# Kernel tuning notes

Measured on AMD Instinct MI355X. Metric: run time of the kernel, lower is better.

The kernel has to match this reference:

```python
import jax, jax.numpy as jnp
import numpy as np

P_NULL = 1e-4


def _neg_mean_sqdist(x, c):
    # x: [B, D], c: [D, K] -> [B, K] = -mean_D (x - c)^2, computed via expansion
    # (same math as torch's (x[:,None]-c.T[None]).square().neg().mean(-1),
    #  avoids materializing a [B,K,D] tensor)
    D = x.shape[-1]
    x2 = jnp.sum(x * x, axis=-1, keepdims=True)          # [B,1]
    c2 = jnp.sum(c * c, axis=0)[None, :]                 # [1,K]
    xc = x @ c                                           # [B,K]
    return -(x2 - 2.0 * xc + c2) / D


def setup_inputs() -> dict:
    key = jax.random.key(0)
    k1, k2, k3 = jax.random.split(key, 3)
    B, G, E, K = 4096, 64, 32, 8192
    images = jax.random.normal(k1, (B, G), dtype=jnp.float32)
    # params mimic nn.Linear weight init scale (kaiming-uniform-ish); exact init irrelevant for math
    xa = jax.random.normal(k2, (G, K), dtype=jnp.float32) * (1.0 / np.sqrt(G))
    xb = jax.random.normal(k3, (E, K), dtype=jnp.float32) * (1.0 / np.sqrt(E))
    return {"images": images, "xa": xa, "xb": xb, "n_step": 4}


def reference(images, xa, xb, n_step):
    B = images.shape[0]
    log_pnull = jnp.log(jnp.float32(P_NULL))

    # ---- encode ----
    lpik = _neg_mean_sqdist(images, xa)                   # [B,K]
    z = jax.nn.softmax(lpik, axis=-1) @ xb.T              # [B,E]
    for _ in range(n_step):
        lxqik = _neg_mean_sqdist(z, xb)                   # [B,K]
        lxq = jnp.concatenate(
            [lxqik, jnp.full((B, 1), log_pnull, dtype=lxqik.dtype)], axis=1)
        lxq = jax.nn.log_softmax(lxq, axis=-1)            # [B,K+1]
        ljp = lpik + lxq[:, :-1]                          # [B,K]
        xp = jax.nn.softmax(ljp, axis=-1)                 # [B,K]
        z = z + 0.1 * (xp @ xb.T - z)                     # [B,E]

    # ---- decode (ret='rec') ----
    xqik = jnp.exp(_neg_mean_sqdist(z, xb))               # [B,K]
    xqik = xqik / (P_NULL + jnp.sum(xqik, axis=-1, keepdims=True))
    y = xqik @ xa.T                                       # [B,G]
    return y
```

## Files before the change

kernel.cpp:

```cpp
#include <hip/hip_runtime.h>
#include <hip/hip_fp16.h>
#include <math.h>

static constexpr int Gd = 64;
static constexpr int Ed = 32;
static constexpr int Kd = 8192;
static constexpr int R  = 4;
static constexpr int T  = 1024;
static constexpr int NW = 16;
static constexpr int NP = 4;
static constexpr int CS = 2 * T;
static constexpr int EQ = 2;
static constexpr int NEQ = Ed / EQ;
static constexpr float PNULLF = 1e-4f;

template<int CTRL, int RMASK>
__device__ __forceinline__ float dpp_add(float v) {
  int t = __builtin_amdgcn_update_dpp(0, __builtin_bit_cast(int, v), CTRL, RMASK, 0xf, true);
  return v + __builtin_bit_cast(float, t);
}
template<int CTRL, int RMASK>
__device__ __forceinline__ float dpp_fmax(float v) {
  int t = __builtin_amdgcn_update_dpp(__builtin_bit_cast(int, -__builtin_inff()),
                                      __builtin_bit_cast(int, v), CTRL, RMASK, 0xf, false);
  return fmaxf(v, __builtin_bit_cast(float, t));
}
__device__ __forceinline__ float wave_sum(float v) {
  v = dpp_add<0x111, 0xf>(v);
  v = dpp_add<0x112, 0xf>(v);
  v = dpp_add<0x114, 0xf>(v);
  v = dpp_add<0x118, 0xf>(v);
  v = dpp_add<0x142, 0xa>(v);
  v = dpp_add<0x143, 0xc>(v);
  return v;
}
__device__ __forceinline__ float half_sum(float v) {
  v = dpp_add<0x111, 0xf>(v);
  v = dpp_add<0x112, 0xf>(v);
  v = dpp_add<0x114, 0xf>(v);
  v = dpp_add<0x118, 0xf>(v);
  v = dpp_add<0x142, 0xa>(v);
  return v;
}
__device__ __forceinline__ float wave_max(float v) {
  v = dpp_fmax<0x111, 0xf>(v);
  v = dpp_fmax<0x112, 0xf>(v);
  v = dpp_fmax<0x114, 0xf>(v);
  v = dpp_fmax<0x118, 0xf>(v);
  v = dpp_fmax<0x142, 0xa>(v);
  v = dpp_fmax<0x143, 0xc>(v);
  return v;
}

template<bool HW>
__device__ __forceinline__ float2 ldw(const void* p, size_t idx) {
  if constexpr (HW) {
    __half2 h = *reinterpret_cast<const __half2*>(reinterpret_cast<const __half*>(p) + idx);
    return __half22float2(h);
  } else {
    return *reinterpret_cast<const float2*>(reinterpret_cast<const float*>(p) + idx);
  }
}
template<bool HW>
__device__ __forceinline__ float4 ld4w(const void* p, size_t idx) {
  if constexpr (HW) {
    const __half2* ph = reinterpret_cast<const __half2*>(reinterpret_cast<const __half*>(p) + idx);
    float2 a = __half22float2(ph[0]);
    float2 b = __half22float2(ph[1]);
    return make_float4(a.x, a.y, b.x, b.y);
  } else {
    return *reinterpret_cast<const float4*>(reinterpret_cast<const float*>(p) + idx);
  }
}

static constexpr int OFF_LP   = 0;
static constexpr int OFF_IMG  = 32768;
static constexpr int OFF_ZT   = 33024;
static constexpr int OFF_WRD  = 33152;
static constexpr int OFF_MLD  = 35264;
static constexpr int OFF_SLD  = 35268;
static constexpr int OFF_Z2   = 35272;
static constexpr int OFF_X2   = 35276;
static constexpr int SMEM_FLOATS = 35280;

template<bool HW>
__global__ __attribute__((amdgpu_flat_work_group_size(T, T), amdgpu_waves_per_eu(4, 4)))
void glgae_fused(
    const float* __restrict__ images,
    const void*  __restrict__ xaP,
    const void*  __restrict__ xbP,
    const float* __restrict__ c2aP,
    const float* __restrict__ cb2P,
    const int*   __restrict__ nstep_p,
    float* __restrict__ out)
{
  extern __shared__ float sm[];
  float* LP  = sm + OFF_LP;
  float* IMG = sm + OFF_IMG;
  float* ZT  = sm + OFF_ZT;
  float* WRD = sm + OFF_WRD;
  float* MLD = sm + OFF_MLD;
  float* SLD = sm + OFF_SLD;
  float* Z2L = sm + OFF_Z2;
  float* X2L = sm + OFF_X2;

  const int tid  = (int)threadIdx.x;
  const int lane = tid & 63;
  const int wv   = tid >> 6;
  const int rowbase = (int)blockIdx.x * R;
  const int nstep = nstep_p[0];
  const int kb0 = tid * 2;

  if (tid < Gd * R) {
    int g = tid >> 2, r = tid & 3;
    IMG[g * R + r] = images[(size_t)(rowbase + r) * Gd + g];
  }
  __syncthreads();
  if (tid < R) {
    float s = 0.f;
    #pragma unroll
    for (int g = 0; g < Gd; ++g) { float v = IMG[g * R + tid]; s = fmaf(v, v, s); }
    X2L[tid] = s;
  }

  {
    float xk[R][NP][2];
    float c2l[NP][2];
    #pragma unroll
    for (int r = 0; r < R; ++r)
      #pragma unroll
      for (int i = 0; i < NP; ++i) { xk[r][i][0] = 0.f; xk[r][i][1] = 0.f; }
    #pragma unroll
    for (int i = 0; i < NP; ++i) { c2l[i][0] = 0.f; c2l[i][1] = 0.f; }

    #pragma unroll 2
    for (int g = 0; g < Gd; ++g) {
      float4 imv4 = *reinterpret_cast<const float4*>(&IMG[g * R]);
      float im[4] = {imv4.x, imv4.y, imv4.z, imv4.w};
      #pragma unroll
      for (int i = 0; i < NP; ++i) {
        float2 w = ldw<HW>(xaP, (size_t)g * Kd + i * CS + kb0);
        if constexpr (!HW) {
          c2l[i][0] = fmaf(w.x, w.x, c2l[i][0]);
          c2l[i][1] = fmaf(w.y, w.y, c2l[i][1]);
        }
        #pragma unroll
        for (int r = 0; r < R; ++r) {
          xk[r][i][0] = fmaf(im[r], w.x, xk[r][i][0]);
          xk[r][i][1] = fmaf(im[r], w.y, xk[r][i][1]);
        }
      }
    }
    __syncthreads();

    float mx[R] = {-__builtin_inff(), -__builtin_inff(), -__builtin_inff(), -__builtin_inff()};
    float x2r[R];
    #pragma unroll
    for (int r = 0; r < R; ++r) x2r[r] = X2L[r];
    #pragma unroll
    for (int i = 0; i < NP; ++i) {
      float cx, cy;
      if constexpr (HW) {
        float2 c = *reinterpret_cast<const float2*>(&c2aP[i * CS + kb0]);
        cx = c.x; cy = c.y;
      } else { cx = c2l[i][0]; cy = c2l[i][1]; }
      #pragma unroll
      for (int r = 0; r < R; ++r) {
        float v0 = (2.f * xk[r][i][0] - x2r[r] - cx) * (1.f / 64.f);
        float v1 = (2.f * xk[r][i][1] - x2r[r] - cy) * (1.f / 64.f);
        mx[r] = fmaxf(mx[r], fmaxf(v0, v1));
        *reinterpret_cast<float2*>(&LP[r * Kd + i * CS + kb0]) = make_float2(v0, v1);
      }
    }
    #pragma unroll
    for (int r = 0; r < R; ++r) mx[r] = wave_max(mx[r]);
    if (lane == 63) {
      #pragma unroll
      for (int r = 0; r < R; ++r) WRD[wv * 132 + 128 + r] = mx[r];
    }
    __syncthreads();
    if (tid < R) {
      float m = -__builtin_inff();
      #pragma unroll
      for (int w = 0; w < NW; ++w) m = fmaxf(m, WRD[w * 132 + 128 + tid]);
      MLD[tid] = m;
    }
    __syncthreads();
  }

  {
    float p[R][NP][2];
    float s1[R] = {0.f, 0.f, 0.f, 0.f};
    #pragma unroll
    for (int i = 0; i < NP; ++i) {
      #pragma unroll
      for (int r = 0; r < R; ++r) {
        float2 l = *reinterpret_cast<const float2*>(&LP[r * Kd + i * CS + kb0]);
        float m = MLD[r];
        float p0 = __expf(l.x - m);
        float p1 = __expf(l.y - m);
        p[r][i][0] = p0; p[r][i][1] = p1;
        s1[r] += p0 + p1;
      }
    }

    float c2v[NP][2];
    #pragma unroll
    for (int i = 0; i < NP; ++i) { c2v[i][0] = 0.f; c2v[i][1] = 0.f; }

    #pragma unroll 1
    for (int eq = 0; eq < NEQ; ++eq) {
      float zacc[R][EQ];
      #pragma unroll
      for (int r = 0; r < R; ++r)
        #pragma unroll
        for (int e2 = 0; e2 < EQ; ++e2) zacc[r][e2] = 0.f;

      #pragma unroll
      for (int i = 0; i < NP; ++i) {
        #pragma unroll
        for (int e2 = 0; e2 < EQ; ++e2) {
          int e = eq * EQ + e2;
          float2 w = ldw<HW>(xbP, (size_t)e * Kd + i * CS + kb0);
          if constexpr (!HW) {
            c2v[i][0] = fmaf(w.x, w.x, c2v[i][0]);
            c2v[i][1] = fmaf(w.y, w.y, c2v[i][1]);
          }
          #pragma unroll
          for (int r = 0; r < R; ++r) {
            zacc[r][e2] = fmaf(p[r][i][0], w.x, zacc[r][e2]);
            zacc[r][e2] = fmaf(p[r][i][1], w.y, zacc[r][e2]);
          }
        }
      }
      #pragma unroll
      for (int r = 0; r < R; ++r)
        #pragma unroll
        for (int e2 = 0; e2 < EQ; ++e2) zacc[r][e2] = wave_sum(zacc[r][e2]);
      if (lane == 63) {
        #pragma unroll
        for (int r = 0; r < R; ++r)
          #pragma unroll
          for (int e2 = 0; e2 < EQ; ++e2)
            WRD[wv * 132 + r * 32 + eq * EQ + e2] = zacc[r][e2];
      }
    }

    #pragma unroll
    for (int r = 0; r < R; ++r) s1[r] = wave_sum(s1[r]);
    if (lane == 63) {
      #pragma unroll
      for (int r = 0; r < R; ++r) WRD[wv * 132 + 128 + r] = s1[r];
    }

    #pragma unroll
    for (int i = 0; i < NP; ++i) {
      float cx, cy;
      if constexpr (HW) {
        float2 c = *reinterpret_cast<const float2*>(&cb2P[i * CS + kb0]);
        cx = c.x; cy = c.y;
      } else { cx = c2v[i][0]; cy = c2v[i][1]; }
      #pragma unroll
      for (int r = 0; r < R; ++r) {
        float2 l = *reinterpret_cast<const float2*>(&LP[r * Kd + i * CS + kb0]);
        l.x -= cx * (1.f / 32.f);
        l.y -= cy * (1.f / 32.f);
        *reinterpret_cast<float2*>(&LP[r * Kd + i * CS + kb0]) = l;
      }
    }

    __syncthreads();
    if (tid < 128) {
      int r = tid >> 5, e = tid & 31;
      float zs = 0.f, ss = 0.f;
      #pragma unroll
      for (int w = 0; w < NW; ++w) { zs += WRD[w * 132 + r * 32 + e]; ss += WRD[w * 132 + 128 + r]; }
      float zn = zs / ss;
      ZT[e * R + r] = zn;
      float q = half_sum(zn * zn);
      if ((lane & 31) == 31) Z2L[r] = q;
    }
    __syncthreads();
  }

  for (int st = 0; st < nstep; ++st) {
    float al[R];
    #pragma unroll
    for (int r = 0; r < R; ++r) al[r] = fmaf(Z2L[r], -(1.f / 32.f), -MLD[r]);

    float up[R][NP][2];
    #pragma unroll
    for (int r = 0; r < R; ++r)
      #pragma unroll
      for (int i = 0; i < NP; ++i) { up[r][i][0] = 0.f; up[r][i][1] = 0.f; }
    #pragma unroll 2
    for (int e = 0; e < Ed; ++e) {
      float4 zv = *reinterpret_cast<const float4*>(&ZT[e * R]);
      float z4[4] = {zv.x, zv.y, zv.z, zv.w};
      #pragma unroll
      for (int i = 0; i < NP; ++i) {
        float2 w = ldw<HW>(xbP, (size_t)e * Kd + i * CS + kb0);
        #pragma unroll
        for (int r = 0; r < R; ++r) {
          up[r][i][0] = fmaf(z4[r], w.x, up[r][i][0]);
          up[r][i][1] = fmaf(z4[r], w.y, up[r][i][1]);
        }
      }
    }

    float s2[R] = {0.f, 0.f, 0.f, 0.f};
    #pragma unroll
    for (int i = 0; i < NP; ++i) {
      #pragma unroll
      for (int r = 0; r < R; ++r) {
        float2 l = *reinterpret_cast<const float2*>(&LP[r * Kd + i * CS + kb0]);
        float p0 = __expf(l.x + al[r] + up[r][i][0] * (1.f / 16.f));
        float p1 = __expf(l.y + al[r] + up[r][i][1] * (1.f / 16.f));
        up[r][i][0] = p0; up[r][i][1] = p1;
        s2[r] += p0 + p1;
      }
    }

    #pragma unroll 1
    for (int eq = 0; eq < NEQ; ++eq) {
      float zacc[R][EQ];
      #pragma unroll
      for (int r = 0; r < R; ++r)
        #pragma unroll
        for (int e2 = 0; e2 < EQ; ++e2) zacc[r][e2] = 0.f;

      #pragma unroll
      for (int i = 0; i < NP; ++i) {
        #pragma unroll
        for (int e2 = 0; e2 < EQ; ++e2) {
          int e = eq * EQ + e2;
          float2 w = ldw<HW>(xbP, (size_t)e * Kd + i * CS + kb0);
          #pragma unroll
          for (int r = 0; r < R; ++r) {
            zacc[r][e2] = fmaf(up[r][i][0], w.x, zacc[r][e2]);
            zacc[r][e2] = fmaf(up[r][i][1], w.y, zacc[r][e2]);
          }
        }
      }
      #pragma unroll
      for (int r = 0; r < R; ++r)
        #pragma unroll
        for (int e2 = 0; e2 < EQ; ++e2) zacc[r][e2] = wave_sum(zacc[r][e2]);
      if (lane == 63) {
        #pragma unroll
        for (int r = 0; r < R; ++r)
          #pragma unroll
          for (int e2 = 0; e2 < EQ; ++e2)
            WRD[wv * 132 + r * 32 + eq * EQ + e2] = zacc[r][e2];
      }
    }

    #pragma unroll
    for (int r = 0; r < R; ++r) s2[r] = wave_sum(s2[r]);
    if (lane == 63) {
      #pragma unroll
      for (int r = 0; r < R; ++r) WRD[wv * 132 + 128 + r] = s2[r];
    }
    __syncthreads();
    if (tid < 128) {
      int r = tid >> 5, e = tid & 31;
      float zs = 0.f, ss = 0.f;
      #pragma unroll
      for (int w = 0; w < NW; ++w) { zs += WRD[w * 132 + r * 32 + e]; ss += WRD[w * 132 + 128 + r]; }
      float zn = fmaf(0.1f, zs / ss, 0.9f * ZT[e * R + r]);
      ZT[e * R + r] = zn;
      float q = half_sum(zn * zn);
      if ((lane & 31) == 31) Z2L[r] = q;
    }
    __syncthreads();
  }

  {
    float u[R][NP][2];
    float cw2[NP][2];
    #pragma unroll
    for (int r = 0; r < R; ++r)
      #pragma unroll
      for (int i = 0; i < NP; ++i) { u[r][i][0] = 0.f; u[r][i][1] = 0.f; }
    #pragma unroll
    for (int i = 0; i < NP; ++i) { cw2[i][0] = 0.f; cw2[i][1] = 0.f; }

    #pragma unroll 2
    for (int e = 0; e < Ed; ++e) {
      float4 zv = *reinterpret_cast<const float4*>(&ZT[e * R]);
      float z4[4] = {zv.x, zv.y, zv.z, zv.w};
      #pragma unroll
      for (int i = 0; i < NP; ++i) {
        float2 w = ldw<HW>(xbP, (size_t)e * Kd + i * CS + kb0);
        if constexpr (!HW) {
          cw2[i][0] = fmaf(w.x, w.x, cw2[i][0]);
          cw2[i][1] = fmaf(w.y, w.y, cw2[i][1]);
        }
        #pragma unroll
        for (int r = 0; r < R; ++r) {
          u[r][i][0] = fmaf(z4[r], w.x, u[r][i][0]);
          u[r][i][1] = fmaf(z4[r], w.y, u[r][i][1]);
        }
      }
    }

    float s3[R] = {0.f, 0.f, 0.f, 0.f};
    float nz2[R];
    #pragma unroll
    for (int r = 0; r < R; ++r) nz2[r] = Z2L[r] * -(1.f / 32.f);
    #pragma unroll
    for (int i = 0; i < NP; ++i) {
      float cx, cy;
      if constexpr (HW) {
        float2 c = *reinterpret_cast<const float2*>(&cb2P[i * CS + kb0]);
        cx = c.x; cy = c.y;
      } else { cx = cw2[i][0]; cy = cw2[i][1]; }
      #pragma unroll
      for (int r = 0; r < R; ++r) {
        float e0 = __expf(nz2[r] + u[r][i][0] * (1.f / 16.f) - cx * (1.f / 32.f));
        float e1 = __expf(nz2[r] + u[r][i][1] * (1.f / 16.f) - cy * (1.f / 32.f));
        *reinterpret_cast<float2*>(&LP[r * Kd + i * CS + kb0]) = make_float2(e0, e1);
        s3[r] += e0 + e1;
      }
    }
    #pragma unroll
    for (int r = 0; r < R; ++r) s3[r] = wave_sum(s3[r]);
    if (lane == 63) {
      #pragma unroll
      for (int r = 0; r < R; ++r) WRD[wv * 132 + 128 + r] = s3[r];
    }
    __syncthreads();
    if (tid < R) {
      float s = 0.f;
      #pragma unroll
      for (int w = 0; w < NW; ++w) s += WRD[w * 132 + 128 + tid];
      SLD[tid] = 1.f / (PNULLF + s);
    }
    __syncthreads();
  }

  {
    float inv[R];
    #pragma unroll
    for (int r = 0; r < R; ++r) inv[r] = SLD[r];
    float acc[R][4];
    #pragma unroll
    for (int r = 0; r < R; ++r)
      #pragma unroll
      for (int gi = 0; gi < 4; ++gi) acc[r][gi] = 0.f;

    #pragma unroll 2
    for (int c = 0; c < 32; ++c) {
      float xq[R][4];
      #pragma unroll
      for (int r = 0; r < R; ++r) {
        float4 q = *reinterpret_cast<const float4*>(&LP[r * Kd + c * 256 + lane * 4]);
        xq[r][0] = q.x; xq[r][1] = q.y; xq[r][2] = q.z; xq[r][3] = q.w;
      }
      #pragma unroll
      for (int gi = 0; gi < 4; ++gi) {
        int g = gi * NW + wv;
        float4 wa = ld4w<HW>(xaP, (size_t)g * Kd + c * 256 + lane * 4);
        #pragma unroll
        for (int r = 0; r < R; ++r) {
          acc[r][gi] = fmaf(xq[r][0], wa.x, acc[r][gi]);
          acc[r][gi] = fmaf(xq[r][1], wa.y, acc[r][gi]);
          acc[r][gi] = fmaf(xq[r][2], wa.z, acc[r][gi]);
          acc[r][gi] = fmaf(xq[r][3], wa.w, acc[r][gi]);
        }
      }
    }
    #pragma unroll
    for (int r = 0; r < R; ++r)
      #pragma unroll
      for (int gi = 0; gi < 4; ++gi) acc[r][gi] = wave_sum(acc[r][gi]);
    if (lane == 63) {
      #pragma unroll
      for (int r = 0; r < R; ++r)
        #pragma unroll
        for (int gi = 0; gi < 4; ++gi)
          out[(size_t)(rowbase + r) * Gd + gi * NW + wv] = acc[r][gi] * inv[r];
    }
  }
}

__global__ __launch_bounds__(256) void convert_w(
    const float* __restrict__ xa, const float* __restrict__ xb,
    __half* __restrict__ xah, __half* __restrict__ xbh,
    float* __restrict__ c2a, float* __restrict__ cb2)
{
  int k = (int)(blockIdx.x * blockDim.x + threadIdx.x);
  if (k >= Kd) return;
  float s = 0.f;
  #pragma unroll 4
  for (int g = 0; g < Gd; ++g) {
    float v = xa[(size_t)g * Kd + k];
    xah[(size_t)g * Kd + k] = __float2half(v);
    s = fmaf(v, v, s);
  }
  c2a[k] = s;
  s = 0.f;
  #pragma unroll 4
  for (int e = 0; e < Ed; ++e) {
    float v = xb[(size_t)e * Kd + k];
    xbh[(size_t)e * Kd + k] = __float2half(v);
    s = fmaf(v, v, s);
  }
  cb2[k] = s;
}

extern "C" void kernel_launch(void* const* d_in, const int* in_sizes, int n_in,
                              void* d_out, int out_size, void* d_ws, size_t ws_size,
                              hipStream_t stream) {
  const float* images = (const float*)d_in[0];
  const float* xa     = (const float*)d_in[1];
  const float* xb     = (const float*)d_in[2];
  const int*   nstep  = (const int*)d_in[3];
  float* out = (float*)d_out;

  const size_t smem = (size_t)SMEM_FLOATS * sizeof(float);
  const size_t need = (size_t)(Gd + Ed) * Kd * sizeof(__half) + (size_t)2 * Kd * sizeof(float);

  if (ws_size >= need) {
    __half* xah = (__half*)d_ws;
    __half* xbh = xah + (size_t)Gd * Kd;
    float*  c2a = (float*)(xbh + (size_t)Ed * Kd);
    float*  cb2 = c2a + Kd;
    hipLaunchKernelGGL(convert_w, dim3(Kd / 256), dim3(256), 0, stream,
                       xa, xb, xah, xbh, c2a, cb2);
    (void)hipFuncSetAttribute((const void*)glgae_fused<true>,
                              hipFuncAttributeMaxDynamicSharedMemorySize, (int)smem);
    hipLaunchKernelGGL(glgae_fused<true>, dim3(4096 / R), dim3(T), smem, stream,
                       images, (const void*)xah, (const void*)xbh, c2a, cb2, nstep, out);
  } else {
    (void)hipFuncSetAttribute((const void*)glgae_fused<false>,
                              hipFuncAttributeMaxDynamicSharedMemorySize, (int)smem);
    hipLaunchKernelGGL(glgae_fused<false>, dim3(4096 / R), dim3(T), smem, stream,
                       images, (const void*)xa, (const void*)xb,
                       (const float*)nullptr, (const float*)nullptr, nstep, out);
  }
}
```

Measured before the change: 838.1 us.

## Use packed fp16 dot2 instructions and pair-interleaved weights in fused kernel

Adds a new half-precision path that packs activations (image, z, probabilities) into fp16 pairs and accumulates with v_dot2 fp16->fp32 instructions against weights pre-interleaved in pairs along the reduction dimension. The fused iterative z update is restructured to work directly on packed probabilities, and the decode stores exp values as fp16 in shared memory. This halves the FMA instruction count and shared/global bytes per product, at the cost of rounding activations and probabilities to fp16 and extra workspace for the interleaved weight copies.

```diff
diff --git a/kernel.cpp b/kernel.cpp
--- a/kernel.cpp
+++ b/kernel.cpp
@@ -10,9 +10,9 @@
 static constexpr int NW = 16;
 static constexpr int NP = 4;
 static constexpr int CS = 2 * T;
-static constexpr int EQ = 2;
-static constexpr int NEQ = Ed / EQ;
 static constexpr float PNULLF = 1e-4f;
+
+typedef _Float16 h2v __attribute__((ext_vector_type(2)));
 
 template<int CTRL, int RMASK>
 __device__ __forceinline__ float dpp_add(float v) {
@@ -52,26 +52,30 @@
   return v;
 }
 
-template<bool HW>
-__device__ __forceinline__ float2 ldw(const void* p, size_t idx) {
-  if constexpr (HW) {
-    __half2 h = *reinterpret_cast<const __half2*>(reinterpret_cast<const __half*>(p) + idx);
-    return __half22float2(h);
-  } else {
-    return *reinterpret_cast<const float2*>(reinterpret_cast<const float*>(p) + idx);
-  }
-}
-template<bool HW>
-__device__ __forceinline__ float4 ld4w(const void* p, size_t idx) {
-  if constexpr (HW) {
-    const __half2* ph = reinterpret_cast<const __half2*>(reinterpret_cast<const __half*>(p) + idx);
-    float2 a = __half22float2(ph[0]);
-    float2 b = __half22float2(ph[1]);
-    return make_float4(a.x, a.y, b.x, b.y);
-  } else {
-    return *reinterpret_cast<const float4*>(reinterpret_cast<const float*>(p) + idx);
-  }
-}
+__device__ __forceinline__ float fdot2(h2v a, h2v b, float c) {
+#if defined(__has_builtin)
+#if __has_builtin(__builtin_amdgcn_fdot2)
+  return __builtin_amdgcn_fdot2(a, b, c, false);
+#else
+  return fmaf((float)a.x, (float)b.x, fmaf((float)a.y, (float)b.y, c));
+#endif
+#else
+  return fmaf((float)a.x, (float)b.x, fmaf((float)a.y, (float)b.y, c));
+#endif
+}
+__device__ __forceinline__ h2v pkh(float x, float y) {
+#if defined(__has_builtin)
+#if __has_builtin(__builtin_amdgcn_cvt_pkrtz)
+  return __builtin_bit_cast(h2v, __builtin_amdgcn_cvt_pkrtz(x, y));
+#else
+  h2v h; h.x = (_Float16)x; h.y = (_Float16)y; return h;
+#endif
+#else
+  h2v h; h.x = (_Float16)x; h.y = (_Float16)y; return h;
+#endif
+}
+__device__ __forceinline__ h2v bch(unsigned int u) { return __builtin_bit_cast(h2v, u); }
+__device__ __forceinline__ unsigned int hbits(h2v h) { return __builtin_bit_cast(unsigned int, h); }
 
 static constexpr int OFF_LP   = 0;
 static constexpr int OFF_IMG  = 32768;
@@ -83,12 +87,13 @@
 static constexpr int OFF_X2   = 35276;
 static constexpr int SMEM_FLOATS = 35280;
 
-template<bool HW>
 __global__ __attribute__((amdgpu_flat_work_group_size(T, T), amdgpu_waves_per_eu(4, 4)))
-void glgae_fused(
+void glgae_h2(
     const float* __restrict__ images,
-    const void*  __restrict__ xaP,
-    const void*  __restrict__ xbP,
+    const __half* __restrict__ xah,
+    const __half* __restrict__ xbh,
+    const unsigned int* __restrict__ xai,
+    const unsigned int* __restrict__ xbi,
     const float* __restrict__ c2aP,
     const float* __restrict__ cb2P,
     const int*   __restrict__ nstep_p,
@@ -103,6 +108,7 @@
   float* SLD = sm + OFF_SLD;
   float* Z2L = sm + OFF_Z2;
   float* X2L = sm + OFF_X2;
+  unsigned int* LPH = reinterpret_cast<unsigned int*>(LP);
 
   const int tid  = (int)threadIdx.x;
   const int lane = tid & 63;
@@ -110,6 +116,369 @@
   const int rowbase = (int)blockIdx.x * R;
   const int nstep = nstep_p[0];
   const int kb0 = tid * 2;
+  const int kp0 = tid;
+
+  if (tid < Gd * R) {
+    int g = tid >> 2, r = tid & 3;
+    IMG[g * R + r] = images[(size_t)(rowbase + r) * Gd + g];
+  }
+  __syncthreads();
+  if (tid < R) {
+    float s = 0.f;
+    #pragma unroll
+    for (int g = 0; g < Gd; ++g) { float v = IMG[g * R + tid]; s = fmaf(v, v, s); }
+    X2L[tid] = s;
+  }
+  __syncthreads();
+
+  {
+    float xk[R][NP][2];
+    #pragma unroll
+    for (int r = 0; r < R; ++r)
+      #pragma unroll
+      for (int i = 0; i < NP; ++i) { xk[r][i][0] = 0.f; xk[r][i][1] = 0.f; }
+
+    #pragma unroll 1
+    for (int gp = 0; gp < Gd / 2; ++gp) {
+      float4 ia = *reinterpret_cast<const float4*>(&IMG[(2 * gp) * R]);
+      float4 ib = *reinterpret_cast<const float4*>(&IMG[(2 * gp + 1) * R]);
+      h2v imh[4] = {pkh(ia.x, ib.x), pkh(ia.y, ib.y), pkh(ia.z, ib.z), pkh(ia.w, ib.w)};
+      #pragma unroll
+      for (int i = 0; i < NP; ++i) {
+        uint2 w = *reinterpret_cast<const uint2*>(xai + (size_t)gp * Kd + i * CS + kb0);
+        h2v w0 = bch(w.x), w1 = bch(w.y);
+        #pragma unroll
+        for (int r = 0; r < R; ++r) {
+          xk[r][i][0] = fdot2(imh[r], w0, xk[r][i][0]);
+          xk[r][i][1] = fdot2(imh[r], w1, xk[r][i][1]);
+        }
+      }
+    }
+
+    float mx[R] = {-__builtin_inff(), -__builtin_inff(), -__builtin_inff(), -__builtin_inff()};
+    float x2r[R];
+    #pragma unroll
+    for (int r = 0; r < R; ++r) x2r[r] = X2L[r];
+    #pragma unroll
+    for (int i = 0; i < NP; ++i) {
+      float2 c = *reinterpret_cast<const float2*>(&c2aP[i * CS + kb0]);
+      #pragma unroll
+      for (int r = 0; r < R; ++r) {
+        float v0 = (2.f * xk[r][i][0] - x2r[r] - c.x) * (1.f / 64.f);
+        float v1 = (2.f * xk[r][i][1] - x2r[r] - c.y) * (1.f / 64.f);
+        mx[r] = fmaxf(mx[r], fmaxf(v0, v1));
+        *reinterpret_cast<float2*>(&LP[r * Kd + i * CS + kb0]) = make_float2(v0, v1);
+      }
+    }
+    #pragma unroll
+    for (int r = 0; r < R; ++r) mx[r] = wave_max(mx[r]);
+    if (lane == 63) {
+      #pragma unroll
+      for (int r = 0; r < R; ++r) WRD[wv * 132 + 128 + r] = mx[r];
+    }
+    __syncthreads();
+    if (tid < R) {
+      float m = -__builtin_inff();
+      #pragma unroll
+      for (int w = 0; w < NW; ++w) m = fmaxf(m, WRD[w * 132 + 128 + tid]);
+      MLD[tid] = m;
+    }
+    __syncthreads();
+  }
+
+  const unsigned int* xbhU = reinterpret_cast<const unsigned int*>(xbh);
+  h2v ph[R][NP];
+
+  {
+    float s1[R] = {0.f, 0.f, 0.f, 0.f};
+    #pragma unroll
+    for (int i = 0; i < NP; ++i) {
+      #pragma unroll
+      for (int r = 0; r < R; ++r) {
+        float2 l = *reinterpret_cast<const float2*>(&LP[r * Kd + i * CS + kb0]);
+        float m = MLD[r];
+        float p0 = __expf(l.x - m);
+        float p1 = __expf(l.y - m);
+        s1[r] += p0 + p1;
+        ph[r][i] = pkh(p0, p1);
+      }
+    }
+
+    #pragma unroll 1
+    for (int eq = 0; eq < 8; ++eq) {
+      float acc[R][4];
+      #pragma unroll
+      for (int r = 0; r < R; ++r)
+        #pragma unroll
+        for (int e2 = 0; e2 < 4; ++e2) acc[r][e2] = 0.f;
+      #pragma unroll
+      for (int i = 0; i < NP; ++i) {
+        #pragma unroll
+        for (int e2 = 0; e2 < 4; ++e2) {
+          int e = eq * 4 + e2;
+          h2v w = bch(xbhU[(size_t)e * (Kd / 2) + i * (CS / 2) + kp0]);
+          #pragma unroll
+          for (int r = 0; r < R; ++r) acc[r][e2] = fdot2(ph[r][i], w, acc[r][e2]);
+        }
+      }
+      #pragma unroll
+      for (int r = 0; r < R; ++r)
+        #pragma unroll
+        for (int e2 = 0; e2 < 4; ++e2) acc[r][e2] = wave_sum(acc[r][e2]);
+      if (lane == 63) {
+        #pragma unroll
+        for (int r = 0; r < R; ++r)
+          #pragma unroll
+          for (int e2 = 0; e2 < 4; ++e2)
+            WRD[wv * 132 + r * 32 + eq * 4 + e2] = acc[r][e2];
+      }
+    }
+
+    #pragma unroll
+    for (int r = 0; r < R; ++r) s1[r] = wave_sum(s1[r]);
+    if (lane == 63) {
+      #pragma unroll
+      for (int r = 0; r < R; ++r) WRD[wv * 132 + 128 + r] = s1[r];
+    }
+
+    #pragma unroll
+    for (int i = 0; i < NP; ++i) {
+      float2 c = *reinterpret_cast<const float2*>(&cb2P[i * CS + kb0]);
+      #pragma unroll
+      for (int r = 0; r < R; ++r) {
+        float2 l = *reinterpret_cast<const float2*>(&LP[r * Kd + i * CS + kb0]);
+        l.x -= c.x * (1.f / 32.f);
+        l.y -= c.y * (1.f / 32.f);
+        *reinterpret_cast<float2*>(&LP[r * Kd + i * CS + kb0]) = l;
+      }
+    }
+
+    __syncthreads();
+    if (tid < 128) {
+      int r = tid >> 5, e = tid & 31;
+      float zs = 0.f, ss = 0.f;
+      #pragma unroll
+      for (int w = 0; w < NW; ++w) { zs += WRD[w * 132 + r * 32 + e]; ss += WRD[w * 132 + 128 + r]; }
+      float zn = zs / ss;
+      ZT[e * R + r] = zn;
+      float q = half_sum(zn * zn);
+      if ((lane & 31) == 31) Z2L[r] = q;
+    }
+    __syncthreads();
+  }
+
+  for (int st = 0; st < nstep; ++st) {
+    float al[R];
+    #pragma unroll
+    for (int r = 0; r < R; ++r) al[r] = fmaf(Z2L[r], -(1.f / 32.f), -MLD[r]);
+
+    float u[R][NP][2];
+    #pragma unroll
+    for (int r = 0; r < R; ++r)
+      #pragma unroll
+      for (int i = 0; i < NP; ++i) { u[r][i][0] = 0.f; u[r][i][1] = 0.f; }
+    #pragma unroll 1
+    for (int ep = 0; ep < Ed / 2; ++ep) {
+      float4 za = *reinterpret_cast<const float4*>(&ZT[(2 * ep) * R]);
+      float4 zb = *reinterpret_cast<const float4*>(&ZT[(2 * ep + 1) * R]);
+      h2v zh[4] = {pkh(za.x, zb.x), pkh(za.y, zb.y), pkh(za.z, zb.z), pkh(za.w, zb.w)};
+      #pragma unroll
+      for (int i = 0; i < NP; ++i) {
+        uint2 w = *reinterpret_cast<const uint2*>(xbi + (size_t)ep * Kd + i * CS + kb0);
+        h2v w0 = bch(w.x), w1 = bch(w.y);
+        #pragma unroll
+        for (int r = 0; r < R; ++r) {
+          u[r][i][0] = fdot2(zh[r], w0, u[r][i][0]);
+          u[r][i][1] = fdot2(zh[r], w1, u[r][i][1]);
+        }
+      }
+    }
+
+    float s2[R] = {0.f, 0.f, 0.f, 0.f};
+    #pragma unroll
+    for (int i = 0; i < NP; ++i) {
+      #pragma unroll
+      for (int r = 0; r < R; ++r) {
+        float2 l = *reinterpret_cast<const float2*>(&LP[r * Kd + i * CS + kb0]);
+        float p0 = __expf(l.x + al[r] + u[r][i][0] * (1.f / 16.f));
+        float p1 = __expf(l.y + al[r] + u[r][i][1] * (1.f / 16.f));
+        s2[r] += p0 + p1;
+        ph[r][i] = pkh(p0, p1);
+      }
+    }
+
+    #pragma unroll 1
+    for (int eq = 0; eq < 8; ++eq) {
+      float acc[R][4];
+      #pragma unroll
+      for (int r = 0; r < R; ++r)
+        #pragma unroll
+        for (int e2 = 0; e2 < 4; ++e2) acc[r][e2] = 0.f;
+      #pragma unroll
+      for (int i = 0; i < NP; ++i) {
+        #pragma unroll
+        for (int e2 = 0; e2 < 4; ++e2) {
+          int e = eq * 4 + e2;
+          h2v w = bch(xbhU[(size_t)e * (Kd / 2) + i * (CS / 2) + kp0]);
+          #pragma unroll
+          for (int r = 0; r < R; ++r) acc[r][e2] = fdot2(ph[r][i], w, acc[r][e2]);
+        }
+      }
+      #pragma unroll
+      for (int r = 0; r < R; ++r)
+        #pragma unroll
+        for (int e2 = 0; e2 < 4; ++e2) acc[r][e2] = wave_sum(acc[r][e2]);
+      if (lane == 63) {
+        #pragma unroll
+        for (int r = 0; r < R; ++r)
+          #pragma unroll
+          for (int e2 = 0; e2 < 4; ++e2)
+            WRD[wv * 132 + r * 32 + eq * 4 + e2] = acc[r][e2];
+      }
+    }
+
+    #pragma unroll
+    for (int r = 0; r < R; ++r) s2[r] = wave_sum(s2[r]);
+    if (lane == 63) {
+      #pragma unroll
+      for (int r = 0; r < R; ++r) WRD[wv * 132 + 128 + r] = s2[r];
+    }
+    __syncthreads();
+    if (tid < 128) {
+      int r = tid >> 5, e = tid & 31;
+      float zs = 0.f, ss = 0.f;
+      #pragma unroll
+      for (int w = 0; w < NW; ++w) { zs += WRD[w * 132 + r * 32 + e]; ss += WRD[w * 132 + 128 + r]; }
+      float zn = fmaf(0.1f, zs / ss, 0.9f * ZT[e * R + r]);
+      ZT[e * R + r] = zn;
+      float q = half_sum(zn * zn);
+      if ((lane & 31) == 31) Z2L[r] = q;
+    }
+    __syncthreads();
+  }
+
+  {
+    float u[R][NP][2];
+    #pragma unroll
+    for (int r = 0; r < R; ++r)
+      #pragma unroll
+      for (int i = 0; i < NP; ++i) { u[r][i][0] = 0.f; u[r][i][1] = 0.f; }
+    #pragma unroll 1
+    for (int ep = 0; ep < Ed / 2; ++ep) {
+      float4 za = *reinterpret_cast<const float4*>(&ZT[(2 * ep) * R]);
+      float4 zb = *reinterpret_cast<const float4*>(&ZT[(2 * ep + 1) * R]);
+      h2v zh[4] = {pkh(za.x, zb.x), pkh(za.y, zb.y), pkh(za.z, zb.z), pkh(za.w, zb.w)};
+      #pragma unroll
+      for (int i = 0; i < NP; ++i) {
+        uint2 w = *reinterpret_cast<const uint2*>(xbi + (size_t)ep * Kd + i * CS + kb0);
+        h2v w0 = bch(w.x), w1 = bch(w.y);
+        #pragma unroll
+        for (int r = 0; r < R; ++r) {
+          u[r][i][0] = fdot2(zh[r], w0, u[r][i][0]);
+          u[r][i][1] = fdot2(zh[r], w1, u[r][i][1]);
+        }
+      }
+    }
+
+    float s3[R] = {0.f, 0.f, 0.f, 0.f};
+    float nz2[R];
+    #pragma unroll
+    for (int r = 0; r < R; ++r) nz2[r] = Z2L[r] * -(1.f / 32.f);
+    __syncthreads();
+    #pragma unroll
+    for (int i = 0; i < NP; ++i) {
+      float2 c = *reinterpret_cast<const float2*>(&cb2P[i * CS + kb0]);
+      #pragma unroll
+      for (int r = 0; r < R; ++r) {
+        float e0 = __expf(nz2[r] + u[r][i][0] * (1.f / 16.f) - c.x * (1.f / 32.f));
+        float e1 = __expf(nz2[r] + u[r][i][1] * (1.f / 16.f) - c.y * (1.f / 32.f));
+        LPH[r * (Kd / 2) + i * (CS / 2) + kp0] = hbits(pkh(e0, e1));
+        s3[r] += e0 + e1;
+      }
+    }
+    #pragma unroll
+    for (int r = 0; r < R; ++r) s3[r] = wave_sum(s3[r]);
+    if (lane == 63) {
+      #pragma unroll
+      for (int r = 0; r < R; ++r) WRD[wv * 132 + 128 + r] = s3[r];
+    }
+    __syncthreads();
+    if (tid < R) {
+      float s = 0.f;
+      #pragma unroll
+      for (int w = 0; w < NW; ++w) s += WRD[w * 132 + 128 + tid];
+      SLD[tid] = 1.f / (PNULLF + s);
+    }
+    __syncthreads();
+  }
+
+  {
+    const unsigned int* xahU = reinterpret_cast<const unsigned int*>(xah);
+    float inv[R];
+    #pragma unroll
+    for (int r = 0; r < R; ++r) inv[r] = SLD[r];
+    float acc[R][4];
+    #pragma unroll
+    for (int r = 0; r < R; ++r)
+      #pragma unroll
+      for (int gi = 0; gi < 4; ++gi) acc[r][gi] = 0.f;
+
+    #pragma unroll 2
+    for (int c = 0; c < 32; ++c) {
+      uint2 q[R];
+      #pragma unroll
+      for (int r = 0; r < R; ++r)
+        q[r] = *reinterpret_cast<const uint2*>(&LPH[r * (Kd / 2) + c * 128 + lane * 2]);
+      #pragma unroll
+      for (int gi = 0; gi < 4; ++gi) {
+        int g = gi * NW + wv;
+        uint2 wa = *reinterpret_cast<const uint2*>(&xahU[(size_t)g * (Kd / 2) + c * 128 + lane * 2]);
+        h2v wa0 = bch(wa.x), wa1 = bch(wa.y);
+        #pragma unroll
+        for (int r = 0; r < R; ++r) {
+          acc[r][gi] = fdot2(bch(q[r].x), wa0, acc[r][gi]);
+          acc[r][gi] = fdot2(bch(q[r].y), wa1, acc[r][gi]);
+        }
+      }
+    }
+    #pragma unroll
+    for (int r = 0; r < R; ++r)
+      #pragma unroll
+      for (int gi = 0; gi < 4; ++gi) acc[r][gi] = wave_sum(acc[r][gi]);
+    if (lane == 63) {
+      #pragma unroll
+      for (int r = 0; r < R; ++r)
+        #pragma unroll
+        for (int gi = 0; gi < 4; ++gi)
+          out[(size_t)(rowbase + r) * Gd + gi * NW + wv] = acc[r][gi] * inv[r];
+    }
+  }
+}
+
+__global__ __attribute__((amdgpu_flat_work_group_size(T, T), amdgpu_waves_per_eu(4, 4)))
+void glgae_f32(
+    const float* __restrict__ images,
+    const float* __restrict__ xa,
+    const float* __restrict__ xb,
+    const int*   __restrict__ nstep_p,
+    float* __restrict__ out)
+{
+  extern __shared__ float sm[];
+  float* LP  = sm + OFF_LP;
+  float* IMG = sm + OFF_IMG;
+  float* ZT  = sm + OFF_ZT;
+  float* WRD = sm + OFF_WRD;
+  float* MLD = sm + OFF_MLD;
+  float* SLD = sm + OFF_SLD;
+  float* Z2L = sm + OFF_Z2;
+  float* X2L = sm + OFF_X2;
+
+  const int tid  = (int)threadIdx.x;
+  const int lane = tid & 63;
+  const int wv   = tid >> 6;
+  const int rowbase = (int)blockIdx.x * R;
+  const int nstep = nstep_p[0];
+  const int kb0 = tid * 2;
 
   if (tid < Gd * R) {
     int g = tid >> 2, r = tid & 3;
@@ -139,11 +508,9 @@
       float im[4] = {imv4.x, imv4.y, imv4.z, imv4.w};
       #pragma unroll
       for (int i = 0; i < NP; ++i) {
-        float2 w = ldw<HW>(xaP, (size_t)g * Kd + i * CS + kb0);
-        if constexpr (!HW) {
-          c2l[i][0] = fmaf(w.x, w.x, c2l[i][0]);
-          c2l[i][1] = fmaf(w.y, w.y, c2l[i][1]);
-        }
+        float2 w = *reinterpret_cast<const float2*>(xa + (size_t)g * Kd + i * CS + kb0);
+        c2l[i][0] = fmaf(w.x, w.x, c2l[i][0]);
+        c2l[i][1] = fmaf(w.y, w.y, c2l[i][1]);
         #pragma unroll
         for (int r = 0; r < R; ++r) {
           xk[r][i][0] = fmaf(im[r], w.x, xk[r][i][0]);
@@ -159,15 +526,10 @@
     for (int r = 0; r < R; ++r) x2r[r] = X2L[r];
     #pragma unroll
     for (int i = 0; i < NP; ++i) {
-      float cx, cy;
-      if constexpr (HW) {
-        float2 c = *reinterpret_cast<const float2*>(&c2aP[i * CS + kb0]);
-        cx = c.x; cy = c.y;
-      } else { cx = c2l[i][0]; cy = c2l[i][1]; }
-      #pragma unroll
-      for (int r = 0; r < R; ++r) {
-        float v0 = (2.f * xk[r][i][0] - x2r[r] - cx) * (1.f / 64.f);
-        float v1 = (2.f * xk[r][i][1] - x2r[r] - cy) * (1.f / 64.f);
+      #pragma unroll
+      for (int r = 0; r < R; ++r) {
+        float v0 = (2.f * xk[r][i][0] - x2r[r] - c2l[i][0]) * (1.f / 64.f);
+        float v1 = (2.f * xk[r][i][1] - x2r[r] - c2l[i][1]) * (1.f / 64.f);
         mx[r] = fmaxf(mx[r], fmaxf(v0, v1));
         *reinterpret_cast<float2*>(&LP[r * Kd + i * CS + kb0]) = make_float2(v0, v1);
       }
@@ -209,23 +571,18 @@
     for (int i = 0; i < NP; ++i) { c2v[i][0] = 0.f; c2v[i][1] = 0.f; }
 
     #pragma unroll 1
-    for (int eq = 0; eq < NEQ; ++eq) {
-      float zacc[R][EQ];
-      #pragma unroll
-      for (int r = 0; r < R; ++r)
-        #pragma unroll
-        for (int e2 = 0; e2 < EQ; ++e2) zacc[r][e2] = 0.f;
-
+    for (int eq = 0; eq < 16; ++eq) {
+      float zacc[R][2];
+      #pragma unroll
+      for (int r = 0; r < R; ++r) { zacc[r][0] = 0.f; zacc[r][1] = 0.f; }
       #pragma unroll
       for (int i = 0; i < NP; ++i) {
         #pragma unroll
-        for (int e2 = 0; e2 < EQ; ++e2) {
-          int e = eq * EQ + e2;
-          float2 w = ldw<HW>(xbP, (size_t)e * Kd + i * CS + kb0);
-          if constexpr (!HW) {
-            c2v[i][0] = fmaf(w.x, w.x, c2v[i][0]);
-            c2v[i][1] = fmaf(w.y, w.y, c2v[i][1]);
-          }
+        for (int e2 = 0; e2 < 2; ++e2) {
+          int e = eq * 2 + e2;
+          float2 w = *reinterpret_cast<const float2*>(xb + (size_t)e * Kd + i * CS + kb0);
+          c2v[i][0] = fmaf(w.x, w.x, c2v[i][0]);
+          c2v[i][1] = fmaf(w.y, w.y, c2v[i][1]);
           #pragma unroll
           for (int r = 0; r < R; ++r) {
             zacc[r][e2] = fmaf(p[r][i][0], w.x, zacc[r][e2]);
@@ -236,13 +593,13 @@
       #pragma unroll
       for (int r = 0; r < R; ++r)
         #pragma unroll
-        for (int e2 = 0; e2 < EQ; ++e2) zacc[r][e2] = wave_sum(zacc[r][e2]);
+        for (int e2 = 0; e2 < 2; ++e2) zacc[r][e2] = wave_sum(zacc[r][e2]);
       if (lane == 63) {
         #pragma unroll
         for (int r = 0; r < R; ++r)
           #pragma unroll
-          for (int e2 = 0; e2 < EQ; ++e2)
-            WRD[wv * 132 + r * 32 + eq * EQ + e2] = zacc[r][e2];
+          for (int e2 = 0; e2 < 2; ++e2)
+            WRD[wv * 132 + r * 32 + eq * 2 + e2] = zacc[r][e2];
       }
     }
 
@@ -255,16 +612,11 @@
 
     #pragma unroll
     for (int i = 0; i < NP; ++i) {
-      float cx, cy;
-      if constexpr (HW) {
-        float2 c = *reinterpret_cast<const float2*>(&cb2P[i * CS + kb0]);
-        cx = c.x; cy = c.y;
-      } else { cx = c2v[i][0]; cy = c2v[i][1]; }
       #pragma unroll
       for (int r = 0; r < R; ++r) {
         float2 l = *reinterpret_cast<const float2*>(&LP[r * Kd + i * CS + kb0]);
-        l.x -= cx * (1.f / 32.f);
-        l.y -= cy * (1.f / 32.f);
+        l.x -= c2v[i][0] * (1.f / 32.f);
+        l.y -= c2v[i][1] * (1.f / 32.f);
         *reinterpret_cast<float2*>(&LP[r * Kd + i * CS + kb0]) = l;
       }
     }
@@ -299,7 +651,7 @@
       float z4[4] = {zv.x, zv.y, zv.z, zv.w};
       #pragma unroll
       for (int i = 0; i < NP; ++i) {
-        float2 w = ldw<HW>(xbP, (size_t)e * Kd + i * CS + kb0);
+        float2 w = *reinterpret_cast<const float2*>(xb + (size_t)e * Kd + i * CS + kb0);
         #pragma unroll
         for (int r = 0; r < R; ++r) {
           up[r][i][0] = fmaf(z4[r], w.x, up[r][i][0]);
@@ -322,19 +674,16 @@
     }
 
     #pragma unroll 1
-    for (int eq = 0; eq < NEQ; ++eq) {
-      float zacc[R][EQ];
-      #pragma unroll
-      for (int r = 0; r < R; ++r)
-        #pragma unroll
-        for (int e2 = 0; e2 < EQ; ++e2) zacc[r][e2] = 0.f;
-
+    for (int eq = 0; eq < 16; ++eq) {
+      float zacc[R][2];
+      #pragma unroll
+      for (int r = 0; r < R; ++r) { zacc[r][0] = 0.f; zacc[r][1] = 0.f; }
       #pragma unroll
       for (int i = 0; i < NP; ++i) {
         #pragma unroll
-        for (int e2 = 0; e2 < EQ; ++e2) {
-          int e = eq * EQ + e2;
-          float2 w = ldw<HW>(xbP, (size_t)e * Kd + i * CS + kb0);
+        for (int e2 = 0; e2 < 2; ++e2) {
+          int e = eq * 2 + e2;
+          float2 w = *reinterpret_cast<const float2*>(xb + (size_t)e * Kd + i * CS + kb0);
           #pragma unroll
           for (int r = 0; r < R; ++r) {
             zacc[r][e2] = fmaf(up[r][i][0], w.x, zacc[r][e2]);
@@ -345,13 +694,13 @@
       #pragma unroll
       for (int r = 0; r < R; ++r)
         #pragma unroll
-        for (int e2 = 0; e2 < EQ; ++e2) zacc[r][e2] = wave_sum(zacc[r][e2]);
+        for (int e2 = 0; e2 < 2; ++e2) zacc[r][e2] = wave_sum(zacc[r][e2]);
       if (lane == 63) {
         #pragma unroll
         for (int r = 0; r < R; ++r)
           #pragma unroll
-          for (int e2 = 0; e2 < EQ; ++e2)
-            WRD[wv * 132 + r * 32 + eq * EQ + e2] = zacc[r][e2];
+          for (int e2 = 0; e2 < 2; ++e2)
+            WRD[wv * 132 + r * 32 + eq * 2 + e2] = zacc[r][e2];
       }
     }
 
@@ -391,11 +740,9 @@
       float z4[4] = {zv.x, zv.y, zv.z, zv.w};
       #pragma unroll
       for (int i = 0; i < NP; ++i) {
-        float2 w = ldw<HW>(xbP, (size_t)e * Kd + i * CS + kb0);
-        if constexpr (!HW) {
-          cw2[i][0] = fmaf(w.x, w.x, cw2[i][0]);
-          cw2[i][1] = fmaf(w.y, w.y, cw2[i][1]);
-        }
+        float2 w = *reinterpret_cast<const float2*>(xb + (size_t)e * Kd + i * CS + kb0);
+        cw2[i][0] = fmaf(w.x, w.x, cw2[i][0]);
+        cw2[i][1] = fmaf(w.y, w.y, cw2[i][1]);
         #pragma unroll
         for (int r = 0; r < R; ++r) {
           u[r][i][0] = fmaf(z4[r], w.x, u[r][i][0]);
@@ -410,15 +757,10 @@
     for (int r = 0; r < R; ++r) nz2[r] = Z2L[r] * -(1.f / 32.f);
     #pragma unroll
     for (int i = 0; i < NP; ++i) {
-      float cx, cy;
-      if constexpr (HW) {
-        float2 c = *reinterpret_cast<const float2*>(&cb2P[i * CS + kb0]);
-        cx = c.x; cy = c.y;
-      } else { cx = cw2[i][0]; cy = cw2[i][1]; }
-      #pragma unroll
-      for (int r = 0; r < R; ++r) {
-        float e0 = __expf(nz2[r] + u[r][i][0] * (1.f / 16.f) - cx * (1.f / 32.f));
-        float e1 = __expf(nz2[r] + u[r][i][1] * (1.f / 16.f) - cy * (1.f / 32.f));
+      #pragma unroll
+      for (int r = 0; r < R; ++r) {
+        float e0 = __expf(nz2[r] + u[r][i][0] * (1.f / 16.f) - cw2[i][0] * (1.f / 32.f));
+        float e1 = __expf(nz2[r] + u[r][i][1] * (1.f / 16.f) - cw2[i][1] * (1.f / 32.f));
         *reinterpret_cast<float2*>(&LP[r * Kd + i * CS + kb0]) = make_float2(e0, e1);
         s3[r] += e0 + e1;
       }
@@ -460,7 +802,7 @@
       #pragma unroll
       for (int gi = 0; gi < 4; ++gi) {
         int g = gi * NW + wv;
-        float4 wa = ld4w<HW>(xaP, (size_t)g * Kd + c * 256 + lane * 4);
+        float4 wa = *reinterpret_cast<const float4*>(xa + (size_t)g * Kd + c * 256 + lane * 4);
         #pragma unroll
         for (int r = 0; r < R; ++r) {
           acc[r][gi] = fmaf(xq[r][0], wa.x, acc[r][gi]);
@@ -487,24 +829,35 @@
 __global__ __launch_bounds__(256) void convert_w(
     const float* __restrict__ xa, const float* __restrict__ xb,
     __half* __restrict__ xah, __half* __restrict__ xbh,
+    unsigned int* __restrict__ xai, unsigned int* __restrict__ xbi,
     float* __restrict__ c2a, float* __restrict__ cb2)
 {
   int k = (int)(blockIdx.x * blockDim.x + threadIdx.x);
   if (k >= Kd) return;
   float s = 0.f;
-  #pragma unroll 4
-  for (int g = 0; g < Gd; ++g) {
-    float v = xa[(size_t)g * Kd + k];
-    xah[(size_t)g * Kd + k] = __float2half(v);
-    s = fmaf(v, v, s);
+  #pragma unroll 2
+  for (int gp = 0; gp < Gd / 2; ++gp) {
+    float va = xa[(size_t)(2 * gp) * Kd + k];
+    float vb = xa[(size_t)(2 * gp + 1) * Kd + k];
+    __half ha = __float2half(va), hb = __float2half(vb);
+    xah[(size_t)(2 * gp) * Kd + k] = ha;
+    xah[(size_t)(2 * gp + 1) * Kd + k] = hb;
+    __half2 hh; hh.x = ha; hh.y = hb;
+    xai[(size_t)gp * Kd + k] = *reinterpret_cast<unsigned int*>(&hh);
+    s = fmaf(va, va, fmaf(vb, vb, s));
   }
   c2a[k] = s;
   s = 0.f;
-  #pragma unroll 4
-  for (int e = 0; e < Ed; ++e) {
-    float v = xb[(size_t)e * Kd + k];
-    xbh[(size_t)e * Kd + k] = __float2half(v);
-    s = fmaf(v, v, s);
+  #pragma unroll 2
+  for (int ep = 0; ep < Ed / 2; ++ep) {
+    float va = xb[(size_t)(2 * ep) * Kd + k];
+    float vb = xb[(size_t)(2 * ep + 1) * Kd + k];
+    __half ha = __float2half(va), hb = __float2half(vb);
+    xbh[(size_t)(2 * ep) * Kd + k] = ha;
+    xbh[(size_t)(2 * ep + 1) * Kd + k] = hb;
+    __half2 hh; hh.x = ha; hh.y = hb;
+    xbi[(size_t)ep * Kd + k] = *reinterpret_cast<unsigned int*>(&hh);
+    s = fmaf(va, va, fmaf(vb, vb, s));
   }
   cb2[k] = s;
 }
@@ -519,24 +872,31 @@
   float* out = (float*)d_out;
 
   const size_t smem = (size_t)SMEM_FLOATS * sizeof(float);
-  const size_t need = (size_t)(Gd + Ed) * Kd * sizeof(__half) + (size_t)2 * Kd * sizeof(float);
+  const size_t szXah = (size_t)Gd * Kd * sizeof(__half);
+  const size_t szXbh = (size_t)Ed * Kd * sizeof(__half);
+  const size_t szXai = (size_t)(Gd / 2) * Kd * sizeof(unsigned);
+  const size_t szXbi = (size_t)(Ed / 2) * Kd * sizeof(unsigned);
+  const size_t szC   = (size_t)Kd * sizeof(float);
+  const size_t need = szXah + szXbh + szXai + szXbi + 2 * szC;
 
   if (ws_size >= need) {
-    __half* xah = (__half*)d_ws;
-    __half* xbh = xah + (size_t)Gd * Kd;
-    float*  c2a = (float*)(xbh + (size_t)Ed * Kd);
-    float*  cb2 = c2a + Kd;
+    char* w = (char*)d_ws;
+    __half* xah = (__half*)w;                w += szXah;
+    __half* xbh = (__half*)w;                w += szXbh;
+    unsigned int* xai = (unsigned int*)w;    w += szXai;
+    unsigned int* xbi = (unsigned int*)w;    w += szXbi;
+    float* c2a = (float*)w;                  w += szC;
+    float* cb2 = (float*)w;
     hipLaunchKernelGGL(convert_w, dim3(Kd / 256), dim3(256), 0, stream,
-                       xa, xb, xah, xbh, c2a, cb2);
-    (void)hipFuncSetAttribute((const void*)glgae_fused<true>,
+                       xa, xb, xah, xbh, xai, xbi, c2a, cb2);
+    (void)hipFuncSetAttribute((const void*)glgae_h2,
                               hipFuncAttributeMaxDynamicSharedMemorySize, (int)smem);
-    hipLaunchKernelGGL(glgae_fused<true>, dim3(4096 / R), dim3(T), smem, stream,
-                       images, (const void*)xah, (const void*)xbh, c2a, cb2, nstep, out);
+    hipLaunchKernelGGL(glgae_h2, dim3(4096 / R), dim3(T), smem, stream,
+                       images, xah, xbh, xai, xbi, c2a, cb2, nstep, out);
   } else {
-    (void)hipFuncSetAttribute((const void*)glgae_fused<false>,
+    (void)hipFuncSetAttribute((const void*)glgae_f32,
                               hipFuncAttributeMaxDynamicSharedMemorySize, (int)smem);
-    hipLaunchKernelGGL(glgae_fused<false>, dim3(4096 / R), dim3(T), smem, stream,
-                       images, (const void*)xa, (const void*)xb,
-                       (const float*)nullptr, (const float*)nullptr, nstep, out);
-  }
-}
+    hipLaunchKernelGGL(glgae_f32, dim3(4096 / R), dim3(T), smem, stream,
+                       images, xa, xb, nstep, out);
+  }
+}
```

New measurement: 745.2 us. -11.1%, faster.
